# Performance work log

Measured on AMD Instinct MI355X. Metric: run time of the kernel, lower is better.

The kernel has to match this reference:

```python
import jax, jax.numpy as jnp
import numpy as np

EMBED_DIM = 2048
NUM_HEADS = 32
HEAD_DIM = EMBED_DIM // NUM_HEADS  # 64
SCALE = HEAD_DIM ** -0.5


def setup_inputs() -> dict:
    key = jax.random.key(0)
    k1, k2, k3, k4, k5 = jax.random.split(key, 5)
    B, S, D = 1, 2048, EMBED_DIM
    return {
        "hidden_states": jax.random.normal(k1, (B, S, D), jnp.float32),
        "w_qkv": jax.random.normal(k2, (3 * D, D), jnp.float32) * (D ** -0.5),
        "b_qkv": jax.random.normal(k3, (3 * D,), jnp.float32) * 0.02,
        "w_out": jax.random.normal(k4, (D, D), jnp.float32) * (D ** -0.5),
        "b_out": jax.random.normal(k5, (D,), jnp.float32) * 0.02,
    }


def reference(hidden_states, w_qkv, b_qkv, w_out, b_out):
    B, S, D = hidden_states.shape
    H, Hd = NUM_HEADS, HEAD_DIM
    # fused QKV projection: [B,S,3D]
    qkv = jnp.einsum("bsd,ed->bse", hidden_states, w_qkv) + b_qkv
    q, k, v = jnp.split(qkv, 3, axis=-1)
    # [B,H,S,Hd]
    q = q.reshape(B, S, H, Hd).transpose(0, 2, 1, 3)
    k = k.reshape(B, S, H, Hd).transpose(0, 2, 1, 3)
    v = v.reshape(B, S, H, Hd).transpose(0, 2, 1, 3)
    scores = jnp.einsum("bhqd,bhkd->bhqk", q, k) * SCALE
    causal = jnp.tril(jnp.ones((S, S), bool))  # [S,S]
    scores = jnp.where(causal, scores, jnp.finfo(scores.dtype).min)
    probs = jax.nn.softmax(scores, axis=-1)
    attn = jnp.einsum("bhqk,bhkd->bhqd", probs, v)
    attn = attn.transpose(0, 2, 1, 3).reshape(B, S, D)
    return jnp.einsum("bsd,ed->bse", attn, w_out) + b_out
```

## Files before the change

kernel.cpp:

```cpp
#include <hip/hip_runtime.h>
#include <hip/hip_bf16.h>

typedef __bf16 bf16;
typedef __attribute__((ext_vector_type(8))) __bf16 bf16x8;
typedef __attribute__((ext_vector_type(4))) float f32x4;

#define S_LEN 2048
#define DM 2048
#define NH 32
#define HD 64
#define QKV_LD 6144
#define SCALE2 0.18033688011112042f
#define DEFER_THR 8.0f

__device__ __forceinline__ float fast_exp2(float x) {
  return __builtin_amdgcn_exp2f(x);
}

__device__ __forceinline__ void gload_lds16(const bf16* g, const bf16* l) {
  __builtin_amdgcn_global_load_lds(
      (const __attribute__((address_space(1))) void*)(uintptr_t)g,
      (__attribute__((address_space(3))) void*)(uint32_t)(uintptr_t)l,
      16, 0, 0);
}

template <int N>
__device__ __forceinline__ void waitcnt_vm() {
  if constexpr (N == 0)      asm volatile("s_waitcnt vmcnt(0)" ::: "memory");
  else if constexpr (N == 4) asm volatile("s_waitcnt vmcnt(4)" ::: "memory");
  else if constexpr (N == 5) asm volatile("s_waitcnt vmcnt(5)" ::: "memory");
  else if constexpr (N == 6) asm volatile("s_waitcnt vmcnt(6)" ::: "memory");
  else if constexpr (N == 7) asm volatile("s_waitcnt vmcnt(7)" ::: "memory");
  else if constexpr (N == 8) asm volatile("s_waitcnt vmcnt(8)" ::: "memory");
  else static_assert(N == 0, "add vmcnt case");
}

template <int CTRL>
__device__ __forceinline__ float fdpp(float x) {
  return __builtin_bit_cast(float,
      __builtin_amdgcn_update_dpp(0, __builtin_bit_cast(int, x), CTRL, 0xF, 0xF, true));
}
__device__ __forceinline__ float red16_max(float x) {
  x = fmaxf(x, fdpp<0xB1>(x));
  x = fmaxf(x, fdpp<0x4E>(x));
  x = fmaxf(x, fdpp<0x141>(x));
  x = fmaxf(x, fdpp<0x140>(x));
  return x;
}
__device__ __forceinline__ float red16_sum(float x) {
  x += fdpp<0xB1>(x);
  x += fdpp<0x4E>(x);
  x += fdpp<0x141>(x);
  x += fdpp<0x140>(x);
  return x;
}

__global__ __launch_bounds__(256) void cvt3_f32_bf16(
    const float* __restrict__ s0, bf16* __restrict__ d0, const int n0,
    const float* __restrict__ s1, bf16* __restrict__ d1, const int n1,
    const float* __restrict__ s2, bf16* __restrict__ d2, const int n2)
{
  const int total = n0 + n1 + n2;
  const int stride = gridDim.x * blockDim.x;
  for (int i = blockIdx.x * blockDim.x + threadIdx.x; i < total; i += stride) {
    const float* s; bf16* d; int j = i;
    if (j < n0)            { s = s0; d = d0; }
    else if (j - n0 < n1)  { s = s1; d = d1; j -= n0; }
    else                   { s = s2; d = d2; j -= n0 + n1; }
    const f32x4 a = *(const f32x4*)(s + (size_t)j * 8);
    const f32x4 b = *(const f32x4*)(s + (size_t)j * 8 + 4);
    bf16x8 r;
    r[0] = (bf16)a[0]; r[1] = (bf16)a[1]; r[2] = (bf16)a[2]; r[3] = (bf16)a[3];
    r[4] = (bf16)b[0]; r[5] = (bf16)b[1]; r[6] = (bf16)b[2]; r[7] = (bf16)b[3];
    *(bf16x8*)(d + (size_t)j * 8) = r;
  }
}

template <int BM, int BN, int WRN, int WCN, int NT, int MINW, typename TO>
__global__ __launch_bounds__(NT, MINW) void gemm_pipe(
    const bf16* __restrict__ A, const bf16* __restrict__ W,
    const float* __restrict__ bias, TO* __restrict__ C,
    const int M, const int N, const int K)
{
  constexpr int WM = BM / WRN, WN = BN / WCN;
  constexpr int MI = WM / 16, NI = WN / 16;
  constexpr int CA = (BM * 64 * 2) / (NT * 16);
  constexpr int CB = (BN * 64 * 2) / (NT * 16);
  constexpr int BUFE = (BM + BN) * 64;
  __shared__ __align__(16) bf16 lds[2 * BUFE];
  const int tid  = threadIdx.x;
  const int lane = tid & 63;
  const int wid  = tid >> 6;
  const int wr = wid / WCN, wc = wid % WCN;
  const int row0 = blockIdx.y * BM, col0 = blockIdx.x * BN;
  const int lq = lane & 15, seg = lane >> 4;

  const f32x4 fz = {0.f, 0.f, 0.f, 0.f};
  f32x4 acc[MI][NI];
#pragma unroll
  for (int i = 0; i < MI; ++i)
#pragma unroll
    for (int j = 0; j < NI; ++j) acc[i][j] = fz;

  auto stage = [&](const int kt, const int b) {
    const int k0 = kt << 6;
    bf16* Ab = lds + b * BUFE;
    bf16* Bb = Ab + BM * 64;
#pragma unroll
    for (int c = 0; c < CA; ++c) {
      const int off16 = c * NT + tid;
      const int row = off16 >> 3;
      const int ch  = (off16 & 7) ^ (row & 7);
      gload_lds16(A + (size_t)(row0 + row) * K + k0 + (ch << 3),
                  Ab + (size_t)(c * NT + (wid << 6)) * 8);
    }
#pragma unroll
    for (int c = 0; c < CB; ++c) {
      const int off16 = c * NT + tid;
      const int row = off16 >> 3;
      const int ch  = (off16 & 7) ^ (row & 7);
      gload_lds16(W + (size_t)(col0 + row) * K + k0 + (ch << 3),
                  Bb + (size_t)(c * NT + (wid << 6)) * 8);
    }
  };

  const int nt = K >> 6;
  stage(0, 0);

  for (int t = 0; t < nt; ++t) {
    asm volatile("" ::: "memory");
    __builtin_amdgcn_s_barrier();
    asm volatile("" ::: "memory");
    if (t + 1 < nt) {
      stage(t + 1, (t + 1) & 1);
      waitcnt_vm<CA + CB>();
    } else {
      waitcnt_vm<0>();
    }
    __builtin_amdgcn_s_barrier();
    asm volatile("" ::: "memory");

    const bf16* Ab = lds + (t & 1) * BUFE;
    const bf16* Bb = Ab + BM * 64;
#pragma unroll
    for (int kk = 0; kk < 2; ++kk) {
      bf16x8 af[MI], bfr[NI];
#pragma unroll
      for (int i = 0; i < MI; ++i) {
        const int row = wr * WM + (i << 4) + lq;
        af[i] = *(const bf16x8*)(Ab + row * 64 +
                 ((((kk << 2) + seg) ^ (row & 7)) << 3));
      }
#pragma unroll
      for (int j = 0; j < NI; ++j) {
        const int row = wc * WN + (j << 4) + lq;
        bfr[j] = *(const bf16x8*)(Bb + row * 64 +
                 ((((kk << 2) + seg) ^ (row & 7)) << 3));
      }
      __builtin_amdgcn_s_setprio(1);
#pragma unroll
      for (int i = 0; i < MI; ++i)
#pragma unroll
        for (int j = 0; j < NI; ++j)
          acc[i][j] = __builtin_amdgcn_mfma_f32_16x16x32_bf16(af[i], bfr[j], acc[i][j], 0, 0, 0);
      __builtin_amdgcn_s_setprio(0);
    }
  }

#pragma unroll
  for (int j = 0; j < NI; ++j) {
    const int col = col0 + wc * WN + (j << 4) + lq;
    const float bv = bias[col];
#pragma unroll
    for (int i = 0; i < MI; ++i) {
      const int rbase = row0 + wr * WM + (i << 4) + (seg << 2);
#pragma unroll
      for (int r = 0; r < 4; ++r)
        C[(size_t)(rbase + r) * N + col] = (TO)(acc[i][j][r] + bv);
    }
  }
}

struct QTile {
  bf16x8 qf[2];
  f32x4  o[4];
  float  m[4], l[4];
};

__device__ __forceinline__ void qtile_init(QTile& st, const bf16* Qg,
                                           const int lq, const int seg) {
  const bf16x8 r0 = *(const bf16x8*)(Qg + (size_t)lq * QKV_LD + seg * 8);
  const bf16x8 r1 = *(const bf16x8*)(Qg + (size_t)lq * QKV_LD + 32 + seg * 8);
#pragma unroll
  for (int j = 0; j < 8; ++j) {
    st.qf[0][j] = (bf16)((float)r0[j] * SCALE2);
    st.qf[1][j] = (bf16)((float)r1[j] * SCALE2);
  }
  const f32x4 fz = {0.f, 0.f, 0.f, 0.f};
#pragma unroll
  for (int r = 0; r < 4; ++r) { st.o[r] = fz; st.m[r] = -1e30f; st.l[r] = 0.f; }
}

__device__ __forceinline__ void qtile_step(
    QTile& st, const int qb, const int nt,
    const int ws, const int lq, const int seg,
    const bf16 (&Ks)[64][64], const bf16 (&Vt)[64][64], bf16 (&Psw)[16][64])
{
  const f32x4 fz = {0.f, 0.f, 0.f, 0.f};
  f32x4 s[4];
  __builtin_amdgcn_s_setprio(1);
#pragma unroll
  for (int ct = 0; ct < 4; ++ct) {
    s[ct] = fz;
#pragma unroll
    for (int ks = 0; ks < 2; ++ks) {
      const int blk = ((ks << 2) + seg) ^ (lq & 7);
      const bf16x8 kf = *(const bf16x8*)(&Ks[(ct << 4) + lq][blk << 3]);
      s[ct] = __builtin_amdgcn_mfma_f32_16x16x32_bf16(st.qf[ks], kf, s[ct], 0, 0, 0);
    }
  }
  __builtin_amdgcn_s_setprio(0);

  if (nt == qb) {
#pragma unroll
    for (int ct = 0; ct < 4; ++ct) {
      const int key = (nt << 6) + (ct << 4) + lq;
#pragma unroll
      for (int r = 0; r < 4; ++r) {
        const int qrow = (qb << 6) + (ws << 4) + (seg << 2) + r;
        if (key > qrow) s[ct][r] = -1e30f;
      }
    }
  }

#pragma unroll
  for (int r = 0; r < 4; ++r) {
    float tm = fmaxf(fmaxf(s[0][r], s[1][r]), fmaxf(s[2][r], s[3][r]));
    tm = red16_max(tm);
    if (tm > st.m[r] + DEFER_THR) {
      const float sc = fast_exp2(st.m[r] - tm);
      st.m[r] = tm;
      st.l[r] *= sc;
#pragma unroll
      for (int dt = 0; dt < 4; ++dt) st.o[dt][r] *= sc;
    }
    float rs = 0.f;
#pragma unroll
    for (int ct = 0; ct < 4; ++ct) {
      const float p = fast_exp2(s[ct][r] - st.m[r]);
      s[ct][r] = p;
      rs += p;
    }
    rs = red16_sum(rs);
    st.l[r] += rs;
  }

#pragma unroll
  for (int ct = 0; ct < 4; ++ct)
#pragma unroll
    for (int r = 0; r < 4; ++r) {
      const int q = (seg << 2) + r;
      const int colp = ((ct << 4) + lq) ^ ((q & 7) << 3);
      Psw[q][colp] = (bf16)s[ct][r];
    }

  __builtin_amdgcn_s_setprio(1);
#pragma unroll
  for (int ks = 0; ks < 2; ++ks) {
    const int blkp = ((ks << 2) + seg) ^ (lq & 7);
    const bf16x8 af = *(const bf16x8*)(&Psw[lq][blkp << 3]);
#pragma unroll
    for (int dt = 0; dt < 4; ++dt) {
      const int xv = (lq & 7) ^ (((dt << 1) + (lq >> 3)) & 7);
      const int blkv = ((ks << 2) + seg) ^ xv;
      const bf16x8 bv = *(const bf16x8*)(&Vt[(dt << 4) + lq][blkv << 3]);
      st.o[dt] = __builtin_amdgcn_mfma_f32_16x16x32_bf16(af, bv, st.o[dt], 0, 0, 0);
    }
  }
  __builtin_amdgcn_s_setprio(0);
}

__device__ __forceinline__ void qtile_store(
    const QTile& st, bf16* __restrict__ out, const int qb, const int h,
    const int ws, const int lq, const int seg)
{
  float rinv[4];
#pragma unroll
  for (int r = 0; r < 4; ++r) rinv[r] = 1.f / st.l[r];
#pragma unroll
  for (int dt = 0; dt < 4; ++dt)
#pragma unroll
    for (int r = 0; r < 4; ++r) {
      const int qrow = (qb << 6) + (ws << 4) + (seg << 2) + r;
      out[(size_t)qrow * DM + h * HD + (dt << 4) + lq] =
          (bf16)(st.o[dt][r] * rinv[r]);
    }
}

__global__ __launch_bounds__(512) void attn_flash(
    const bf16* __restrict__ qkv, bf16* __restrict__ out)
{
  __shared__ __align__(16) bf16 Ks[64][64];
  __shared__ __align__(16) bf16 Vt[64][64];
  __shared__ __align__(16) bf16 Ps[8][16][64];
  const int qbA = blockIdx.x;
  const int qbB = 31 - qbA;
  const int h   = blockIdx.y;
  const int tid = threadIdx.x;
  const int lane = tid & 63, wid = tid >> 6;
  const int lq = lane & 15, seg = lane >> 4;
  const int myqb = (wid < 4) ? qbA : qbB;
  const int ws   = wid & 3;

  const bf16* Kg = qkv + DM + h * HD;
  const bf16* Vg = qkv + 2 * DM + h * HD;

  QTile st;
  qtile_init(st, qkv + (size_t)(myqb * 64 + ws * 16) * QKV_LD + h * HD, lq, seg);

  const int srow = tid >> 3, sch = tid & 7;

  bf16x8 kr = *(const bf16x8*)(Kg + (size_t)srow * QKV_LD + (sch << 3));
  bf16x8 vr = *(const bf16x8*)(Vg + (size_t)srow * QKV_LD + (sch << 3));

  for (int nt = 0; nt <= qbB; ++nt) {
    __syncthreads();
    *(bf16x8*)(&Ks[srow][(sch ^ (srow & 7)) << 3]) = kr;
#pragma unroll
    for (int j = 0; j < 8; ++j) {
      const int keyp = srow ^ ((j ^ sch) << 3);
      Vt[(sch << 3) + j][keyp] = vr[j];
    }
    __syncthreads();

    if (nt < qbB) {
      const int row = ((nt + 1) << 6) + srow;
      kr = *(const bf16x8*)(Kg + (size_t)row * QKV_LD + (sch << 3));
      vr = *(const bf16x8*)(Vg + (size_t)row * QKV_LD + (sch << 3));
    }

    if (nt <= myqb)
      qtile_step(st, myqb, nt, ws, lq, seg, Ks, Vt, Ps[wid]);
  }

  qtile_store(st, out, myqb, h, ws, lq, seg);
}

extern "C" void kernel_launch(void* const* d_in, const int* in_sizes, int n_in,
                              void* d_out, int out_size, void* d_ws, size_t ws_size,
                              hipStream_t stream) {
  (void)in_sizes; (void)n_in; (void)out_size; (void)ws_size;
  const float* hidden = (const float*)d_in[0];
  const float* w_qkv  = (const float*)d_in[1];
  const float* b_qkv  = (const float*)d_in[2];
  const float* w_out  = (const float*)d_in[3];
  const float* b_out  = (const float*)d_in[4];
  float* out = (float*)d_out;

  bf16* qkvbuf  = (bf16*)d_ws;
  bf16* attnbuf = qkvbuf  + (size_t)S_LEN * (3 * DM);
  bf16* hidb    = attnbuf + (size_t)S_LEN * DM;
  bf16* wqkvb   = hidb    + (size_t)S_LEN * DM;
  bf16* woutb   = wqkvb   + (size_t)(3 * DM) * DM;

  dim3 blk(256);
  cvt3_f32_bf16<<<dim3(2048), blk, 0, stream>>>(
      hidden, hidb, (S_LEN * DM) / 8,
      w_qkv, wqkvb, (3 * DM * DM) / 8,
      w_out, woutb, (DM * DM) / 8);
  gemm_pipe<128, 192, 2, 4, 512, 4, bf16><<<dim3(32, 16), dim3(512), 0, stream>>>(
      hidb, wqkvb, b_qkv, qkvbuf, S_LEN, 3 * DM, DM);
  attn_flash<<<dim3(16, NH), dim3(512), 0, stream>>>(qkvbuf, attnbuf);
  gemm_pipe<64, 128, 1, 4, 256, 2, float><<<dim3(16, 32), dim3(256), 0, stream>>>(
      attnbuf, woutb, b_out, out, S_LEN, DM, DM);
}
```

Baseline: 148.9 us.

## Double-buffer K/V tiles in attention and remap blocks per XCD

The attention kernel now keeps two LDS buffers for K and V, so the next tile is written into the alternate buffer after computing on the current one. This removes one of the two barriers per iteration. The launch becomes a 1D grid whose block index is decoded so that the heads sharing an XCD stay together, aiming at better L2 reuse of K/V. Launch bounds now request 4 blocks per CU, which may cap registers, and the larger LDS footprint could limit occupancy.

```diff
diff --git a/kernel.cpp b/kernel.cpp
--- a/kernel.cpp
+++ b/kernel.cpp
@@ -297,15 +297,17 @@
     }
 }
 
-__global__ __launch_bounds__(512) void attn_flash(
+__global__ __launch_bounds__(512, 4) void attn_flash(
     const bf16* __restrict__ qkv, bf16* __restrict__ out)
 {
-  __shared__ __align__(16) bf16 Ks[64][64];
-  __shared__ __align__(16) bf16 Vt[64][64];
+  __shared__ __align__(16) bf16 Ks[2][64][64];
+  __shared__ __align__(16) bf16 Vt[2][64][64];
   __shared__ __align__(16) bf16 Ps[8][16][64];
-  const int qbA = blockIdx.x;
+  const int bid = blockIdx.x;
+  const int xcd = bid & 7, idx = bid >> 3;
+  const int h   = (xcd << 2) | (idx >> 4);
+  const int qbA = idx & 15;
   const int qbB = 31 - qbA;
-  const int h   = blockIdx.y;
   const int tid = threadIdx.x;
   const int lane = tid & 63, wid = tid >> 6;
   const int lq = lane & 15, seg = lane >> 4;
@@ -320,19 +322,18 @@
 
   const int srow = tid >> 3, sch = tid & 7;
 
-  bf16x8 kr = *(const bf16x8*)(Kg + (size_t)srow * QKV_LD + (sch << 3));
-  bf16x8 vr = *(const bf16x8*)(Vg + (size_t)srow * QKV_LD + (sch << 3));
+  {
+    const bf16x8 k0 = *(const bf16x8*)(Kg + (size_t)srow * QKV_LD + (sch << 3));
+    const bf16x8 v0 = *(const bf16x8*)(Vg + (size_t)srow * QKV_LD + (sch << 3));
+    *(bf16x8*)(&Ks[0][srow][(sch ^ (srow & 7)) << 3]) = k0;
+#pragma unroll
+    for (int j = 0; j < 8; ++j)
+      Vt[0][(sch << 3) + j][srow ^ ((j ^ sch) << 3)] = v0[j];
+  }
+  __syncthreads();
 
   for (int nt = 0; nt <= qbB; ++nt) {
-    __syncthreads();
-    *(bf16x8*)(&Ks[srow][(sch ^ (srow & 7)) << 3]) = kr;
-#pragma unroll
-    for (int j = 0; j < 8; ++j) {
-      const int keyp = srow ^ ((j ^ sch) << 3);
-      Vt[(sch << 3) + j][keyp] = vr[j];
-    }
-    __syncthreads();
-
+    bf16x8 kr, vr;
     if (nt < qbB) {
       const int row = ((nt + 1) << 6) + srow;
       kr = *(const bf16x8*)(Kg + (size_t)row * QKV_LD + (sch << 3));
@@ -340,7 +341,16 @@
     }
 
     if (nt <= myqb)
-      qtile_step(st, myqb, nt, ws, lq, seg, Ks, Vt, Ps[wid]);
+      qtile_step(st, myqb, nt, ws, lq, seg, Ks[nt & 1], Vt[nt & 1], Ps[wid]);
+
+    if (nt < qbB) {
+      const int b = (nt + 1) & 1;
+      *(bf16x8*)(&Ks[b][srow][(sch ^ (srow & 7)) << 3]) = kr;
+#pragma unroll
+      for (int j = 0; j < 8; ++j)
+        Vt[b][(sch << 3) + j][srow ^ ((j ^ sch) << 3)] = vr[j];
+    }
+    __syncthreads();
   }
 
   qtile_store(st, out, myqb, h, ws, lq, seg);
@@ -370,7 +380,7 @@
       w_out, woutb, (DM * DM) / 8);
   gemm_pipe<128, 192, 2, 4, 512, 4, bf16><<<dim3(32, 16), dim3(512), 0, stream>>>(
       hidb, wqkvb, b_qkv, qkvbuf, S_LEN, 3 * DM, DM);
-  attn_flash<<<dim3(16, NH), dim3(512), 0, stream>>>(qkvbuf, attnbuf);
+  attn_flash<<<dim3(512), dim3(512), 0, stream>>>(qkvbuf, attnbuf);
   gemm_pipe<64, 128, 1, 4, 256, 2, float><<<dim3(16, 32), dim3(256), 0, stream>>>(
       attnbuf, woutb, b_out, out, S_LEN, DM, DM);
 }
```

After: 147.9 us, median of 2. Within noise of the previous version (-0.7%).
